# Kernel tuning notes

Hardware: AMD Instinct MI355X
Metric: run time of the kernel (lower is better)

The kernel has to match this reference:

```python
import jax, jax.numpy as jnp
import numpy as np
import math

B, S, H = 2, 2048, 1024
NH = 16
HD = H // NH  # 64


def setup_inputs() -> dict:
    key = jax.random.key(0)
    ks = jax.random.split(key, 8)
    scale = 1.0 / math.sqrt(H)
    inp = {
        "hidden_states": jax.random.normal(ks[0], (B, S, H), dtype=jnp.float32),
        "attention_mask": jnp.zeros((B, 1, 1, S), dtype=jnp.float32),
        "Wq": jax.random.normal(ks[1], (H, H), dtype=jnp.float32) * scale,
        "bq": jnp.zeros((H,), dtype=jnp.float32),
        "Wk": jax.random.normal(ks[2], (H, H), dtype=jnp.float32) * scale,
        "bk": jnp.zeros((H,), dtype=jnp.float32),
        "Wv": jax.random.normal(ks[3], (H, H), dtype=jnp.float32) * scale,
        "bv": jnp.zeros((H,), dtype=jnp.float32),
    }
    return inp


def reference(hidden_states, attention_mask, Wq, bq, Wk, bk, Wv, bv):
    # torch Linear: y = x @ W.T + b; W is (out, in)
    def split_heads(x):  # [B,S,H] -> [B,NH,S,HD]
        return x.reshape(B, S, NH, HD).transpose(0, 2, 1, 3)

    q = split_heads(hidden_states @ Wq.T + bq)
    k = split_heads(hidden_states @ Wk.T + bk)
    v = split_heads(hidden_states @ Wv.T + bv)

    scores = jnp.einsum('bhqd,bhkd->bhqk', q, k) / jnp.sqrt(jnp.float32(HD))
    scores = scores + attention_mask  # additive mask, broadcast [B,1,1,S]
    probs = jax.nn.softmax(scores, axis=-1)
    # dropout prob = 0.0 -> identity
    ctx = jnp.einsum('bhqk,bhkd->bhqd', probs, v)
    ctx = ctx.transpose(0, 2, 1, 3).reshape(B, S, H)
    return ctx
```

## Files before the change

kernel.cpp:

```cpp
#include <hip/hip_runtime.h>
#include <hip/hip_bf16.h>
#include <stdint.h>

constexpr int cB = 2;
constexpr int cS = 2048;
constexpr int cH = 1024;
constexpr int cNH = 16;
constexpr int cHD = 64;
constexpr int cBS = cB * cS;

typedef short short8 __attribute__((ext_vector_type(8)));
typedef short short4v __attribute__((ext_vector_type(4)));
typedef float f32x4 __attribute__((ext_vector_type(4)));
typedef unsigned short us4 __attribute__((ext_vector_type(4)));

constexpr float LOG2E = 1.4426950408889634f;

__device__ inline unsigned short f2bf(float f) {
  __hip_bfloat16 h = __float2bfloat16(f);
  return __builtin_bit_cast(unsigned short, h);
}

__device__ inline float fexp2(float x) {
#if __has_builtin(__builtin_amdgcn_exp2f)
  return __builtin_amdgcn_exp2f(x);
#else
  return __expf(x * 0.6931471805599453f);
#endif
}

__device__ inline void gload_lds16(const void* g, void* l) {
  __builtin_amdgcn_global_load_lds(
      (const __attribute__((address_space(1))) void*)g,
      (__attribute__((address_space(3))) void*)l,
      16, 0, 0);
}

__device__ inline short4v tr16(const unsigned short* p) {
  short4v d;
  auto p3 = (const __attribute__((address_space(3))) unsigned short*)p;
  asm volatile("ds_read_b64_tr_b16 %0, %1" : "=v"(d) : "v"(p3) : "memory");
  return d;
}

template <int CTRL>
__device__ inline float dppmax(float x) {
  int v = __builtin_bit_cast(int, x);
  int y = __builtin_amdgcn_update_dpp(0, v, CTRL, 0xf, 0xf, true);
  return fmaxf(x, __builtin_bit_cast(float, y));
}

__device__ inline float rowmax16(float x) {
  x = dppmax<0x121>(x);
  x = dppmax<0x122>(x);
  x = dppmax<0x124>(x);
  x = dppmax<0x128>(x);
  return x;
}

__global__ void cvt_f32_bf16(const float* __restrict__ src,
                             unsigned short* __restrict__ dst, int n) {
  int i = (blockIdx.x * blockDim.x + threadIdx.x) * 4;
  if (i >= n) return;
  f32x4 v = *reinterpret_cast<const f32x4*>(src + i);
  us4 o = {f2bf(v[0]), f2bf(v[1]), f2bf(v[2]), f2bf(v[3])};
  *reinterpret_cast<us4*>(dst + i) = o;
}

constexpr int BM = 128, BN = 128, BK = 32;

__global__ __launch_bounds__(256) void qkv_gemm(
    const unsigned short* __restrict__ Xb,
    const unsigned short* __restrict__ Wqb,
    const unsigned short* __restrict__ Wkb,
    const unsigned short* __restrict__ Wvb,
    const float* __restrict__ bq, const float* __restrict__ bk,
    const float* __restrict__ bv,
    unsigned short* __restrict__ Qb, unsigned short* __restrict__ Kb,
    unsigned short* __restrict__ Vb) {
  __shared__ alignas(16) unsigned short As[BM * BK];
  __shared__ alignas(16) unsigned short Bs[BN * BK];

  const int nb = blockIdx.x;
  const int mb = blockIdx.y;
  const int m0 = mb * BM;
  const int wsel = nb >> 3;
  const int n0 = (nb & 7) * BN;
  const unsigned short* W = (wsel == 0) ? Wqb : (wsel == 1 ? Wkb : Wvb);
  const float* bias = (wsel == 0) ? bq : (wsel == 1 ? bk : bv);
  unsigned short* Out = (wsel == 0) ? Qb : (wsel == 1 ? Kb : Vb);
  const float oscale = (wsel == 0) ? 0.125f * LOG2E : 1.0f;

  const int t = threadIdx.x;
  const int w = t >> 6, l = t & 63, lr = l & 15, lg = l >> 4;
  const int wm = w >> 1, wn = w & 1;

  f32x4 acc[4][4];
#pragma unroll
  for (int mi = 0; mi < 4; ++mi)
#pragma unroll
    for (int ni = 0; ni < 4; ++ni) acc[mi][ni] = {0.f, 0.f, 0.f, 0.f};

  const int tb = t * 16;

  for (int kt = 0; kt < cH / BK; ++kt) {
    const int k0 = kt * BK;
    __syncthreads();
#pragma unroll
    for (int s = 0; s < 2; ++s) {
      const int ib = s * 4096 + tb;
      const int row = ib >> 6;
      const int cole = (ib & 63) >> 1;
      gload_lds16(Xb + (size_t)(m0 + row) * cH + k0 + cole,
                  ((char*)As) + s * 4096 + w * 1024);
      gload_lds16(W + (size_t)(n0 + row) * cH + k0 + cole,
                  ((char*)Bs) + s * 4096 + w * 1024);
    }
    asm volatile("s_waitcnt vmcnt(0)" ::: "memory");
    __syncthreads();

    short8 af[4], bfr[4];
#pragma unroll
    for (int mi = 0; mi < 4; ++mi)
      af[mi] = *reinterpret_cast<const short8*>(
          &As[(wm * 64 + mi * 16 + lr) * BK + lg * 8]);
#pragma unroll
    for (int ni = 0; ni < 4; ++ni)
      bfr[ni] = *reinterpret_cast<const short8*>(
          &Bs[(wn * 64 + ni * 16 + lr) * BK + lg * 8]);
#pragma unroll
    for (int mi = 0; mi < 4; ++mi)
#pragma unroll
      for (int ni = 0; ni < 4; ++ni)
        acc[mi][ni] = __builtin_amdgcn_mfma_f32_16x16x32_bf16(
            af[mi], bfr[ni], acc[mi][ni], 0, 0, 0);
  }

#pragma unroll
  for (int ni = 0; ni < 4; ++ni) {
    const int col = n0 + wn * 64 + ni * 16 + lr;
    const float bvv = bias[col];
#pragma unroll
    for (int mi = 0; mi < 4; ++mi) {
      const int row = m0 + wm * 64 + mi * 16 + lg * 4;
#pragma unroll
      for (int r = 0; r < 4; ++r)
        Out[(size_t)(row + r) * cH + col] =
            f2bf((acc[mi][ni][r] + bvv) * oscale);
    }
  }
}

__global__ __launch_bounds__(256) void attn_kernel(
    const unsigned short* __restrict__ Qb,
    const unsigned short* __restrict__ Kb,
    const unsigned short* __restrict__ Vb,
    const float* __restrict__ mask,
    float* __restrict__ out) {
  __shared__ alignas(16) unsigned short Ks[2][64 * 64];
  __shared__ alignas(16) unsigned short Vs[2][64 * 64];
  __shared__ alignas(16) unsigned short plds[4][2][64 * 16];

  const int qb = blockIdx.x;
  const int bh = blockIdx.y;
  const int b = bh >> 4, h = bh & 15;
  const int t = threadIdx.x;
  const int w = t >> 6, l = t & 63, lr = l & 15, lg = l >> 4;
  const int q0 = qb * 128 + w * 32;

  const unsigned short* Kbase = Kb + (size_t)b * cS * cH + h * cHD;
  const unsigned short* Vbase = Vb + (size_t)b * cS * cH + h * cHD;
  const float* mbase = mask + b * cS;

  int rK[2], cK[2], rV[2], cV[2];
#pragma unroll
  for (int s2 = 0; s2 < 2; ++s2) {
    const int g = (w * 2 + s2) * 64 + l;
    const int gr = g >> 3, gc = g & 7;
    rK[s2] = gr;
    cK[s2] = (gc ^ (gr & 7)) * 8;
    rV[s2] = (gr >> 2) * 4 + (gc >> 1);
    cV[s2] = (gr & 3) * 16 + (gc & 1) * 8;
  }

  short8 qf[2][2];
#pragma unroll
  for (int qi = 0; qi < 2; ++qi) {
    const unsigned short* Qrow =
        Qb + (size_t)(b * cS + q0 + qi * 16 + lr) * cH + h * cHD;
    qf[qi][0] = *reinterpret_cast<const short8*>(Qrow + lg * 8);
    qf[qi][1] = *reinterpret_cast<const short8*>(Qrow + 32 + lg * 8);
  }

  short8 ones;
#pragma unroll
  for (int j = 0; j < 8; ++j) ones[j] = (short)0x3F80;

  f32x4 oacc[2][4];
  f32x4 osum[2];
  float mrow[2][4];
#pragma unroll
  for (int qi = 0; qi < 2; ++qi) {
    osum[qi] = {0.f, 0.f, 0.f, 0.f};
#pragma unroll
    for (int d16 = 0; d16 < 4; ++d16) oacc[qi][d16] = {0.f, 0.f, 0.f, 0.f};
#pragma unroll
    for (int r = 0; r < 4; ++r) mrow[qi][r] = -1e30f;
  }

  auto stage = [&](int bufi, int kv0) {
#pragma unroll
    for (int s2 = 0; s2 < 2; ++s2) {
      gload_lds16(Kbase + (size_t)(kv0 + rK[s2]) * cH + cK[s2],
                  (char*)&Ks[bufi][0] + (w * 2 + s2) * 1024);
      gload_lds16(Vbase + (size_t)(kv0 + rV[s2]) * cH + cV[s2],
                  (char*)&Vs[bufi][0] + (w * 2 + s2) * 1024);
    }
  };

  stage(0, 0);
  asm volatile("s_waitcnt vmcnt(0)" ::: "memory");
  __syncthreads();

  unsigned short* pw0 = &plds[w][0][0];
  unsigned short* pw1 = &plds[w][1][0];

  constexpr int NT = cS / 64;
  for (int kt = 0; kt < NT; ++kt) {
    const int bufi = kt & 1;
    if (kt + 1 < NT) stage(bufi ^ 1, (kt + 1) * 64);

    const unsigned short* Kt = &Ks[bufi][0];
    const unsigned short* Vt = &Vs[bufi][0];
    const int kv0 = kt * 64;

    float mv[4];
#pragma unroll
    for (int n = 0; n < 4; ++n) mv[n] = mbase[kv0 + n * 16 + lr] * LOG2E;

    f32x4 sc[2][4];
#pragma unroll
    for (int n = 0; n < 4; ++n) {
      const int kr = n * 16 + lr;
      const unsigned sw = (unsigned)((kr & 7) << 4);
      const unsigned b0 = ((unsigned)(kr * 128 + lg * 16)) ^ sw;
      const unsigned b1 = ((unsigned)(kr * 128 + 64 + lg * 16)) ^ sw;
      short8 kf0 = *reinterpret_cast<const short8*>((const char*)Kt + b0);
      short8 kf1 = *reinterpret_cast<const short8*>((const char*)Kt + b1);
#pragma unroll
      for (int qi = 0; qi < 2; ++qi) {
        f32x4 z = {0.f, 0.f, 0.f, 0.f};
        z = __builtin_amdgcn_mfma_f32_16x16x32_bf16(qf[qi][0], kf0, z, 0, 0, 0);
        z = __builtin_amdgcn_mfma_f32_16x16x32_bf16(qf[qi][1], kf1, z, 0, 0, 0);
        sc[qi][n] = z + mv[n];
      }
    }

    float mnew[2][4];
    int ok = 1;
#pragma unroll
    for (int qi = 0; qi < 2; ++qi)
#pragma unroll
      for (int r = 0; r < 4; ++r) {
        float mx = fmaxf(fmaxf(sc[qi][0][r], sc[qi][1][r]),
                         fmaxf(sc[qi][2][r], sc[qi][3][r]));
        mx = rowmax16(mx);
        mnew[qi][r] = fmaxf(mrow[qi][r], mx);
        ok &= (mx - mrow[qi][r] <= 11.5416f) ? 1 : 0;
      }
    if (!__all(ok)) {
#pragma unroll
      for (int qi = 0; qi < 2; ++qi) {
#pragma unroll
        for (int r = 0; r < 4; ++r) {
          const float scalef = fexp2(mrow[qi][r] - mnew[qi][r]);
          mrow[qi][r] = mnew[qi][r];
          osum[qi][r] *= scalef;
#pragma unroll
          for (int d16 = 0; d16 < 4; ++d16) oacc[qi][d16][r] *= scalef;
        }
      }
    }

#pragma unroll
    for (int qi = 0; qi < 2; ++qi) {
      unsigned short* pw = qi ? pw1 : pw0;
      const int pcb = (lg ^ (lr >> 2)) * 4;
#pragma unroll
      for (int n = 0; n < 4; ++n) {
        short4v v4;
#pragma unroll
        for (int r = 0; r < 4; ++r)
          v4[r] = (short)f2bf(fexp2(sc[qi][n][r] - mrow[qi][r]));
        *reinterpret_cast<short4v*>(&pw[(n * 16 + lr) * 16 + pcb]) = v4;
      }
    }
    asm volatile("s_waitcnt lgkmcnt(0)" ::: "memory");
    __builtin_amdgcn_sched_barrier(0);

    short4v pt[2][4];
    short4v tv[2][8];
#pragma unroll
    for (int ks2 = 0; ks2 < 2; ++ks2) {
      const int k0 = ks2 * 32 + lg * 8;
      const int key = (lg & 1) * 2;
      pt[ks2][0] = tr16(&pw0[(k0 + (lr >> 2)) * 16 + (((lr & 3) ^ key) * 4)]);
      pt[ks2][1] =
          tr16(&pw0[(k0 + 4 + (lr >> 2)) * 16 + (((lr & 3) ^ key ^ 1) * 4)]);
      pt[ks2][2] = tr16(&pw1[(k0 + (lr >> 2)) * 16 + (((lr & 3) ^ key) * 4)]);
      pt[ks2][3] =
          tr16(&pw1[(k0 + 4 + (lr >> 2)) * 16 + (((lr & 3) ^ key ^ 1) * 4)]);
#pragma unroll
      for (int d16 = 0; d16 < 4; ++d16) {
        const unsigned short* a0 =
            Vt + (ks2 * 8 + lg * 2) * 256 + d16 * 64 + lr * 4;
        tv[ks2][2 * d16] = tr16(a0);
        tv[ks2][2 * d16 + 1] = tr16(a0 + 256);
      }
    }
    asm volatile("s_waitcnt lgkmcnt(0)" ::: "memory");
    __builtin_amdgcn_sched_barrier(0);
#pragma unroll
    for (int ks2 = 0; ks2 < 2; ++ks2) {
      short8 paA, paB;
#pragma unroll
      for (int j = 0; j < 4; ++j) {
        paA[j] = pt[ks2][0][j];
        paA[4 + j] = pt[ks2][1][j];
        paB[j] = pt[ks2][2][j];
        paB[4 + j] = pt[ks2][3][j];
      }
      osum[0] =
          __builtin_amdgcn_mfma_f32_16x16x32_bf16(paA, ones, osum[0], 0, 0, 0);
      osum[1] =
          __builtin_amdgcn_mfma_f32_16x16x32_bf16(paB, ones, osum[1], 0, 0, 0);
#pragma unroll
      for (int d16 = 0; d16 < 4; ++d16) {
        short8 vf;
#pragma unroll
        for (int j = 0; j < 4; ++j) {
          vf[j] = tv[ks2][2 * d16][j];
          vf[4 + j] = tv[ks2][2 * d16 + 1][j];
        }
        oacc[0][d16] = __builtin_amdgcn_mfma_f32_16x16x32_bf16(
            paA, vf, oacc[0][d16], 0, 0, 0);
        oacc[1][d16] = __builtin_amdgcn_mfma_f32_16x16x32_bf16(
            paB, vf, oacc[1][d16], 0, 0, 0);
      }
    }

    asm volatile("s_waitcnt vmcnt(0)" ::: "memory");
    __syncthreads();
  }

#pragma unroll
  for (int qi = 0; qi < 2; ++qi) {
    float* obase =
        out + (size_t)(b * cS + q0 + qi * 16 + lg * 4) * cH + h * cHD;
#pragma unroll
    for (int r = 0; r < 4; ++r) {
      const float inv = 1.0f / osum[qi][r];
#pragma unroll
      for (int d16 = 0; d16 < 4; ++d16)
        obase[(size_t)r * cH + d16 * 16 + lr] = oacc[qi][d16][r] * inv;
    }
  }
}

extern "C" void kernel_launch(void* const* d_in, const int* in_sizes, int n_in,
                              void* d_out, int out_size, void* d_ws,
                              size_t ws_size, hipStream_t stream) {
  const float* X = (const float*)d_in[0];
  const float* mask = (const float*)d_in[1];
  const float* Wq = (const float*)d_in[2];
  const float* bq = (const float*)d_in[3];
  const float* Wk = (const float*)d_in[4];
  const float* bk = (const float*)d_in[5];
  const float* Wv = (const float*)d_in[6];
  const float* bv = (const float*)d_in[7];
  float* outp = (float*)d_out;

  char* ws = (char*)d_ws;
  const size_t MB = 1 << 20;
  unsigned short* Xb  = (unsigned short*)(ws + 0 * MB);
  unsigned short* Wqb = (unsigned short*)(ws + 8 * MB);
  unsigned short* Wkb = (unsigned short*)(ws + 10 * MB);
  unsigned short* Wvb = (unsigned short*)(ws + 12 * MB);
  unsigned short* Qb  = (unsigned short*)(ws + 14 * MB);
  unsigned short* Kb  = (unsigned short*)(ws + 22 * MB);
  unsigned short* Vb  = (unsigned short*)(ws + 30 * MB);

  cvt_f32_bf16<<<cBS * cH / 1024, 256, 0, stream>>>(X, Xb, cBS * cH);
  cvt_f32_bf16<<<cH * cH / 1024, 256, 0, stream>>>(Wq, Wqb, cH * cH);
  cvt_f32_bf16<<<cH * cH / 1024, 256, 0, stream>>>(Wk, Wkb, cH * cH);
  cvt_f32_bf16<<<cH * cH / 1024, 256, 0, stream>>>(Wv, Wvb, cH * cH);

  qkv_gemm<<<dim3(24, 32), 256, 0, stream>>>(Xb, Wqb, Wkb, Wvb, bq, bk, bv,
                                             Qb, Kb, Vb);
  attn_kernel<<<dim3(16, 32), 256, 0, stream>>>(Qb, Kb, Vb, mask, outp);
}
```

Baseline: 135.4 us.

## Compute transposed scores and build P operand in registers instead of LDS

Swaps the MFMA operand order so scores come out as K-by-Q, which puts one query row per lane. The row max then needs only two cross-lane shuffles, and the mask loads become vector loads. The P operand for the PV MFMA is now assembled in registers with permlane32 swaps and shuffles, so the per-wave LDS write, wait and transposed-read round trip is gone. The cost is extra shuffle instructions, per-row rescale broadcasts through __shfl, and higher register pressure from keeping all K fragments live.

```diff
diff --git a/kernel.cpp b/kernel.cpp
--- a/kernel.cpp
+++ b/kernel.cpp
@@ -13,6 +13,7 @@
 typedef short short4v __attribute__((ext_vector_type(4)));
 typedef float f32x4 __attribute__((ext_vector_type(4)));
 typedef unsigned short us4 __attribute__((ext_vector_type(4)));
+typedef unsigned uint4v __attribute__((ext_vector_type(4)));
 
 constexpr float LOG2E = 1.4426950408889634f;
 
@@ -43,19 +44,8 @@
   return d;
 }
 
-template <int CTRL>
-__device__ inline float dppmax(float x) {
-  int v = __builtin_bit_cast(int, x);
-  int y = __builtin_amdgcn_update_dpp(0, v, CTRL, 0xf, 0xf, true);
-  return fmaxf(x, __builtin_bit_cast(float, y));
-}
-
-__device__ inline float rowmax16(float x) {
-  x = dppmax<0x121>(x);
-  x = dppmax<0x122>(x);
-  x = dppmax<0x124>(x);
-  x = dppmax<0x128>(x);
-  return x;
+__device__ inline void swap32(unsigned& a, unsigned& b) {
+  asm("v_permlane32_swap_b32 %0, %1" : "+v"(a), "+v"(b));
 }
 
 __global__ void cvt_f32_bf16(const float* __restrict__ src,
@@ -159,7 +149,6 @@
     float* __restrict__ out) {
   __shared__ alignas(16) unsigned short Ks[2][64 * 64];
   __shared__ alignas(16) unsigned short Vs[2][64 * 64];
-  __shared__ alignas(16) unsigned short plds[4][2][64 * 16];
 
   const int qb = blockIdx.x;
   const int bh = blockIdx.y;
@@ -171,6 +160,10 @@
   const unsigned short* Kbase = Kb + (size_t)b * cS * cH + h * cHD;
   const unsigned short* Vbase = Vb + (size_t)b * cS * cH + h * cHD;
   const float* mbase = mask + b * cS;
+
+  const int sel = (l >> 4) & 1;
+  const int idxm16 = l - 16;
+  const int idxp16 = (l + 16) & 63;
 
   int rK[2], cK[2], rV[2], cV[2];
 #pragma unroll
@@ -198,14 +191,13 @@
 
   f32x4 oacc[2][4];
   f32x4 osum[2];
-  float mrow[2][4];
+  float mrow[2];
 #pragma unroll
   for (int qi = 0; qi < 2; ++qi) {
     osum[qi] = {0.f, 0.f, 0.f, 0.f};
 #pragma unroll
     for (int d16 = 0; d16 < 4; ++d16) oacc[qi][d16] = {0.f, 0.f, 0.f, 0.f};
-#pragma unroll
-    for (int r = 0; r < 4; ++r) mrow[qi][r] = -1e30f;
+    mrow[qi] = -1e30f;
   }
 
   auto stage = [&](int bufi, int kv0) {
@@ -222,9 +214,6 @@
   asm volatile("s_waitcnt vmcnt(0)" ::: "memory");
   __syncthreads();
 
-  unsigned short* pw0 = &plds[w][0][0];
-  unsigned short* pw1 = &plds[w][1][0];
-
   constexpr int NT = cS / 64;
   for (int kt = 0; kt < NT; ++kt) {
     const int bufi = kt & 1;
@@ -234,82 +223,20 @@
     const unsigned short* Vt = &Vs[bufi][0];
     const int kv0 = kt * 64;
 
-    float mv[4];
-#pragma unroll
-    for (int n = 0; n < 4; ++n) mv[n] = mbase[kv0 + n * 16 + lr] * LOG2E;
-
-    f32x4 sc[2][4];
+    short8 kfs[4][2];
 #pragma unroll
     for (int n = 0; n < 4; ++n) {
       const int kr = n * 16 + lr;
       const unsigned sw = (unsigned)((kr & 7) << 4);
       const unsigned b0 = ((unsigned)(kr * 128 + lg * 16)) ^ sw;
       const unsigned b1 = ((unsigned)(kr * 128 + 64 + lg * 16)) ^ sw;
-      short8 kf0 = *reinterpret_cast<const short8*>((const char*)Kt + b0);
-      short8 kf1 = *reinterpret_cast<const short8*>((const char*)Kt + b1);
-#pragma unroll
-      for (int qi = 0; qi < 2; ++qi) {
-        f32x4 z = {0.f, 0.f, 0.f, 0.f};
-        z = __builtin_amdgcn_mfma_f32_16x16x32_bf16(qf[qi][0], kf0, z, 0, 0, 0);
-        z = __builtin_amdgcn_mfma_f32_16x16x32_bf16(qf[qi][1], kf1, z, 0, 0, 0);
-        sc[qi][n] = z + mv[n];
-      }
-    }
-
-    float mnew[2][4];
-    int ok = 1;
-#pragma unroll
-    for (int qi = 0; qi < 2; ++qi)
-#pragma unroll
-      for (int r = 0; r < 4; ++r) {
-        float mx = fmaxf(fmaxf(sc[qi][0][r], sc[qi][1][r]),
-                         fmaxf(sc[qi][2][r], sc[qi][3][r]));
-        mx = rowmax16(mx);
-        mnew[qi][r] = fmaxf(mrow[qi][r], mx);
-        ok &= (mx - mrow[qi][r] <= 11.5416f) ? 1 : 0;
-      }
-    if (!__all(ok)) {
-#pragma unroll
-      for (int qi = 0; qi < 2; ++qi) {
-#pragma unroll
-        for (int r = 0; r < 4; ++r) {
-          const float scalef = fexp2(mrow[qi][r] - mnew[qi][r]);
-          mrow[qi][r] = mnew[qi][r];
-          osum[qi][r] *= scalef;
-#pragma unroll
-          for (int d16 = 0; d16 < 4; ++d16) oacc[qi][d16][r] *= scalef;
-        }
-      }
-    }
-
-#pragma unroll
-    for (int qi = 0; qi < 2; ++qi) {
-      unsigned short* pw = qi ? pw1 : pw0;
-      const int pcb = (lg ^ (lr >> 2)) * 4;
-#pragma unroll
-      for (int n = 0; n < 4; ++n) {
-        short4v v4;
-#pragma unroll
-        for (int r = 0; r < 4; ++r)
-          v4[r] = (short)f2bf(fexp2(sc[qi][n][r] - mrow[qi][r]));
-        *reinterpret_cast<short4v*>(&pw[(n * 16 + lr) * 16 + pcb]) = v4;
-      }
-    }
-    asm volatile("s_waitcnt lgkmcnt(0)" ::: "memory");
-    __builtin_amdgcn_sched_barrier(0);
-
-    short4v pt[2][4];
+      kfs[n][0] = *reinterpret_cast<const short8*>((const char*)Kt + b0);
+      kfs[n][1] = *reinterpret_cast<const short8*>((const char*)Kt + b1);
+    }
+
     short4v tv[2][8];
 #pragma unroll
-    for (int ks2 = 0; ks2 < 2; ++ks2) {
-      const int k0 = ks2 * 32 + lg * 8;
-      const int key = (lg & 1) * 2;
-      pt[ks2][0] = tr16(&pw0[(k0 + (lr >> 2)) * 16 + (((lr & 3) ^ key) * 4)]);
-      pt[ks2][1] =
-          tr16(&pw0[(k0 + 4 + (lr >> 2)) * 16 + (((lr & 3) ^ key ^ 1) * 4)]);
-      pt[ks2][2] = tr16(&pw1[(k0 + (lr >> 2)) * 16 + (((lr & 3) ^ key) * 4)]);
-      pt[ks2][3] =
-          tr16(&pw1[(k0 + 4 + (lr >> 2)) * 16 + (((lr & 3) ^ key ^ 1) * 4)]);
+    for (int ks2 = 0; ks2 < 2; ++ks2)
 #pragma unroll
       for (int d16 = 0; d16 < 4; ++d16) {
         const unsigned short* a0 =
@@ -317,23 +244,100 @@
         tv[ks2][2 * d16] = tr16(a0);
         tv[ks2][2 * d16 + 1] = tr16(a0 + 256);
       }
-    }
+
+    f32x4 maskv[4];
+#pragma unroll
+    for (int n = 0; n < 4; ++n) {
+      f32x4 m = *reinterpret_cast<const f32x4*>(&mbase[kv0 + n * 16 + lg * 4]);
+#pragma unroll
+      for (int r = 0; r < 4; ++r) m[r] *= LOG2E;
+      maskv[n] = m;
+    }
+
+    f32x4 sc[2][4];
+#pragma unroll
+    for (int n = 0; n < 4; ++n)
+#pragma unroll
+      for (int qi = 0; qi < 2; ++qi) {
+        f32x4 z = {0.f, 0.f, 0.f, 0.f};
+        z = __builtin_amdgcn_mfma_f32_16x16x32_bf16(kfs[n][0], qf[qi][0], z, 0, 0, 0);
+        z = __builtin_amdgcn_mfma_f32_16x16x32_bf16(kfs[n][1], qf[qi][1], z, 0, 0, 0);
+        sc[qi][n] = z + maskv[n];
+      }
+
+    float mnew[2];
+    int ok = 1;
+#pragma unroll
+    for (int qi = 0; qi < 2; ++qi) {
+      float a0 = fmaxf(fmaxf(sc[qi][0][0], sc[qi][0][1]),
+                       fmaxf(sc[qi][0][2], sc[qi][0][3]));
+      float a1 = fmaxf(fmaxf(sc[qi][1][0], sc[qi][1][1]),
+                       fmaxf(sc[qi][1][2], sc[qi][1][3]));
+      float a2 = fmaxf(fmaxf(sc[qi][2][0], sc[qi][2][1]),
+                       fmaxf(sc[qi][2][2], sc[qi][2][3]));
+      float a3 = fmaxf(fmaxf(sc[qi][3][0], sc[qi][3][1]),
+                       fmaxf(sc[qi][3][2], sc[qi][3][3]));
+      float mx = fmaxf(fmaxf(a0, a1), fmaxf(a2, a3));
+      mx = fmaxf(mx, __shfl_xor(mx, 16));
+      mx = fmaxf(mx, __shfl_xor(mx, 32));
+      mnew[qi] = fmaxf(mrow[qi], mx);
+      ok &= (mx - mrow[qi] <= 11.5416f) ? 1 : 0;
+    }
+    if (!__all(ok)) {
+#pragma unroll
+      for (int qi = 0; qi < 2; ++qi) {
+        const float dlt = mrow[qi] - mnew[qi];
+        mrow[qi] = mnew[qi];
+#pragma unroll
+        for (int r = 0; r < 4; ++r) {
+          const float s = fexp2(__shfl(dlt, lg * 4 + r));
+          osum[qi][r] *= s;
+#pragma unroll
+          for (int d16 = 0; d16 < 4; ++d16) oacc[qi][d16][r] *= s;
+        }
+      }
+    }
+
+    unsigned d0[2][4], d1[2][4];
+#pragma unroll
+    for (int qi = 0; qi < 2; ++qi)
+#pragma unroll
+      for (int n = 0; n < 4; ++n) {
+        const float p0 = fexp2(sc[qi][n][0] - mrow[qi]);
+        const float p1 = fexp2(sc[qi][n][1] - mrow[qi]);
+        const float p2 = fexp2(sc[qi][n][2] - mrow[qi]);
+        const float p3 = fexp2(sc[qi][n][3] - mrow[qi]);
+        d0[qi][n] = (unsigned)f2bf(p0) | ((unsigned)f2bf(p1) << 16);
+        d1[qi][n] = (unsigned)f2bf(p2) | ((unsigned)f2bf(p3) << 16);
+      }
+
     asm volatile("s_waitcnt lgkmcnt(0)" ::: "memory");
     __builtin_amdgcn_sched_barrier(0);
 #pragma unroll
     for (int ks2 = 0; ks2 < 2; ++ks2) {
-      short8 paA, paB;
-#pragma unroll
-      for (int j = 0; j < 4; ++j) {
-        paA[j] = pt[ks2][0][j];
-        paA[4 + j] = pt[ks2][1][j];
-        paB[j] = pt[ks2][2][j];
-        paB[4 + j] = pt[ks2][3][j];
-      }
-      osum[0] =
-          __builtin_amdgcn_mfma_f32_16x16x32_bf16(paA, ones, osum[0], 0, 0, 0);
-      osum[1] =
-          __builtin_amdgcn_mfma_f32_16x16x32_bf16(paB, ones, osum[1], 0, 0, 0);
+      const int a = ks2 * 2;
+      short8 pa[2];
+#pragma unroll
+      for (int qi = 0; qi < 2; ++qi) {
+        unsigned A0 = d0[qi][a], B0 = d0[qi][a + 1];
+        unsigned A1 = d1[qi][a], B1 = d1[qi][a + 1];
+        swap32(A0, B0);
+        swap32(A1, B1);
+        const unsigned sB0 = (unsigned)__shfl((int)B0, idxm16);
+        const unsigned sA0 = (unsigned)__shfl((int)A0, idxp16);
+        const unsigned sB1 = (unsigned)__shfl((int)B1, idxm16);
+        const unsigned sA1 = (unsigned)__shfl((int)A1, idxp16);
+        const unsigned j01 = sel ? sB0 : A0;
+        const unsigned j45 = sel ? B0 : sA0;
+        const unsigned j23 = sel ? sB1 : A1;
+        const unsigned j67 = sel ? B1 : sA1;
+        uint4v q4 = {j01, j23, j45, j67};
+        pa[qi] = __builtin_bit_cast(short8, q4);
+      }
+      osum[0] = __builtin_amdgcn_mfma_f32_16x16x32_bf16(pa[0], ones, osum[0],
+                                                        0, 0, 0);
+      osum[1] = __builtin_amdgcn_mfma_f32_16x16x32_bf16(pa[1], ones, osum[1],
+                                                        0, 0, 0);
 #pragma unroll
       for (int d16 = 0; d16 < 4; ++d16) {
         short8 vf;
@@ -343,9 +347,9 @@
           vf[4 + j] = tv[ks2][2 * d16 + 1][j];
         }
         oacc[0][d16] = __builtin_amdgcn_mfma_f32_16x16x32_bf16(
-            paA, vf, oacc[0][d16], 0, 0, 0);
+            pa[0], vf, oacc[0][d16], 0, 0, 0);
         oacc[1][d16] = __builtin_amdgcn_mfma_f32_16x16x32_bf16(
-            paB, vf, oacc[1][d16], 0, 0, 0);
+            pa[1], vf, oacc[1][d16], 0, 0, 0);
       }
     }
 
```

After: 126.7 us, median of 2. 1.07x faster.
